# Optimization experiments

Hardware: AMD Instinct MI355X
Metric: run time of the kernel (lower is better)

## Reference

```python
import jax, jax.numpy as jnp
import numpy as np

VOCAB = 32000
HID = 512
T_IN = 128
T_OUT = 128
BATCH = 32


def gru_scan(xs, h0, W, U, bi, br):
    """Keras GRUCell (reset_after=True) over time.
    xs: [T, B, H] inputs; h0: [B, H]; W: [H, 3H]; U: [H, 3H]; bi, br: [3H].
    Returns (h_final [B,H], hs [T,B,H])."""
    # input projections for all timesteps at once
    x_proj = jnp.einsum('tbh,hg->tbg', xs, W) + bi  # [T, B, 3H]

    def step(h, xp):
        rec = h @ U + br                      # [B, 3H]
        xz, xr, xh = jnp.split(xp, 3, axis=-1)
        rz, rr, rh = jnp.split(rec, 3, axis=-1)
        z = jax.nn.sigmoid(xz + rz)
        r = jax.nn.sigmoid(xr + rr)
        hh = jnp.tanh(xh + r * rh)
        h_new = z * h + (1.0 - z) * hh
        return h_new, h_new

    h_final, hs = jax.lax.scan(step, h0, x_proj)
    return h_final, hs


def setup_inputs() -> dict:
    key = jax.random.key(0)
    ks = jax.random.split(key, 12)
    s = 0.05
    return {
        'inputs': jax.random.randint(ks[0], (BATCH, T_IN), 0, VOCAB, dtype=jnp.int64 if jax.config.jax_enable_x64 else jnp.int32),
        'emb': jax.random.normal(ks[1], (VOCAB, HID), jnp.float32) * s,
        'enc_W': jax.random.normal(ks[2], (HID, 3 * HID), jnp.float32) * s,
        'enc_U': jax.random.normal(ks[3], (HID, 3 * HID), jnp.float32) * s,
        'enc_bi': jnp.zeros((3 * HID,), jnp.float32),
        'enc_br': jnp.zeros((3 * HID,), jnp.float32),
        'dec_W': jax.random.normal(ks[4], (HID, 3 * HID), jnp.float32) * s,
        'dec_U': jax.random.normal(ks[5], (HID, 3 * HID), jnp.float32) * s,
        'dec_bi': jnp.zeros((3 * HID,), jnp.float32),
        'dec_br': jnp.zeros((3 * HID,), jnp.float32),
        'w_relu': jax.random.normal(ks[6], (HID, HID), jnp.float32) * s,
        'b_relu': jnp.zeros((HID,), jnp.float32),
        'w_out': jax.random.normal(ks[7], (HID, VOCAB), jnp.float32) * s,
        'b_out': jnp.zeros((VOCAB,), jnp.float32),
    }


def reference(inputs, emb, enc_W, enc_U, enc_bi, enc_br,
              dec_W, dec_U, dec_bi, dec_br, w_relu, b_relu, w_out, b_out):
    B = inputs.shape[0]
    # Embedding lookup: [B, T_in, H] -> time-major [T_in, B, H]
    x = jnp.transpose(emb[inputs], (1, 0, 2))
    h0 = jnp.zeros((B, HID), jnp.float32)
    # Encoder GRU -> final state
    h_enc, _ = gru_scan(x, h0, enc_W, enc_U, enc_bi, enc_br)
    # RepeatVector: decoder input is encoder state at every target step
    dec_in = jnp.broadcast_to(h_enc[None], (T_OUT, B, HID))
    # Decoder GRU with fresh zero state, return sequences
    _, hs = gru_scan(dec_in, h0, dec_W, dec_U, dec_bi, dec_br)  # [T_out, B, H]
    hs = jnp.transpose(hs, (1, 0, 2))  # [B, T_out, H]
    # TimeDistributed Dense+relu, then Dense+softmax over vocab
    h1 = jax.nn.relu(jnp.einsum('bth,hk->btk', hs, w_relu) + b_relu)
    logits = jnp.einsum('bth,hv->btv', h1, w_out) + b_out
    return jax.nn.softmax(logits, axis=-1)
```

## Files before the change

### kernel.cpp

```cpp
#include <hip/hip_runtime.h>
#include <stdint.h>

#define VOCAB 32000
#define HID   512
#define G3    1536
#define TT    128
#define BB    32
#define NROW  4096
#define NCB   250

typedef __attribute__((ext_vector_type(8))) short short8;
typedef __attribute__((ext_vector_type(4))) short short4v;
typedef __attribute__((ext_vector_type(4))) float f32x4;
typedef __attribute__((ext_vector_type(2))) unsigned long long u64x2;

__device__ __forceinline__ unsigned short f2bf(float f) {
  unsigned int u = __builtin_bit_cast(unsigned int, f);
  u += 0x7fffu + ((u >> 16) & 1u);
  return (unsigned short)(u >> 16);
}

__device__ __forceinline__ float bf2f(unsigned short s) {
  unsigned int u = ((unsigned int)s) << 16;
  return __builtin_bit_cast(float, u);
}

__device__ __forceinline__ void gload16(const void* g, void* l) {
  __builtin_amdgcn_global_load_lds(
      (const __attribute__((address_space(1))) unsigned int*)g,
      (__attribute__((address_space(3))) unsigned int*)l, 16, 0, 0);
}

__global__ void convert_bf16_k(const float* __restrict__ src,
                               unsigned short* __restrict__ dst, int n) {
  int i = (blockIdx.x * blockDim.x + threadIdx.x) * 8;
  int stride = gridDim.x * blockDim.x * 8;
  for (; i < n; i += stride) {
    float4 a = *(const float4*)(src + i);
    float4 b = *(const float4*)(src + i + 4);
    short8 o;
    o[0] = (short)f2bf(a.x); o[1] = (short)f2bf(a.y);
    o[2] = (short)f2bf(a.z); o[3] = (short)f2bf(a.w);
    o[4] = (short)f2bf(b.x); o[5] = (short)f2bf(b.y);
    o[6] = (short)f2bf(b.z); o[7] = (short)f2bf(b.w);
    *(short8*)(dst + i) = o;
  }
}

__global__ void transpose_bf16_k(const float* __restrict__ src,
                                 unsigned short* __restrict__ dst,
                                 int K, int N) {
  __shared__ float t[64][65];
  int k0 = blockIdx.x * 64, n0 = blockIdx.y * 64;
  int c = threadIdx.x & 15, rr = threadIdx.x >> 4;
#pragma unroll
  for (int i = 0; i < 4; ++i) {
    float4 v = *(const float4*)(src + (size_t)(k0 + rr + 16 * i) * N + n0 + c * 4);
    t[rr + 16 * i][c * 4 + 0] = v.x;
    t[rr + 16 * i][c * 4 + 1] = v.y;
    t[rr + 16 * i][c * 4 + 2] = v.z;
    t[rr + 16 * i][c * 4 + 3] = v.w;
  }
  __syncthreads();
#pragma unroll
  for (int i = 0; i < 4; ++i) {
    short4v o;
#pragma unroll
    for (int j = 0; j < 4; ++j) o[j] = (short)f2bf(t[c * 4 + j][rr + 16 * i]);
    *(short4v*)(dst + (size_t)(n0 + rr + 16 * i) * K + k0 + c * 4) = o;
  }
}

__global__ void embed_k(const int* __restrict__ inputs,
                        const float* __restrict__ emb,
                        unsigned short* __restrict__ xb) {
  int r = blockIdx.x;
  int t = r >> 5, b = r & 31;
  int idx = inputs[b * TT + t];
  const float* src = emb + (size_t)idx * HID;
  unsigned short* dst = xb + (size_t)r * HID;
  int j = threadIdx.x * 4;
  float4 v = *(const float4*)(src + j);
  short4v o;
  o[0] = (short)f2bf(v.x); o[1] = (short)f2bf(v.y);
  o[2] = (short)f2bf(v.z); o[3] = (short)f2bf(v.w);
  *(short4v*)(dst + j) = o;
}

template<int MODE>
__launch_bounds__(256)
__global__ void gemm_bt(const unsigned short* __restrict__ A,
                        const unsigned short* __restrict__ BT,
                        const float* __restrict__ bias,
                        void* __restrict__ Cv,
                        float* __restrict__ partials,
                        int M, int N, int K) {
  __shared__ unsigned short As[8192];
  __shared__ unsigned short Bs[8192];
  __shared__ float rsum[2][128];
  int tid = threadIdx.x;
  int l = tid & 63;
  int w = tid >> 6;
  int wm = w >> 1, wn = w & 1;

  int nwg = (int)(gridDim.x * gridDim.y);
  int id = (int)(blockIdx.y * gridDim.x + blockIdx.x);
  int nid = (id & 7) * (nwg >> 3) + (id >> 3);
  int bx = nid & 31, by = nid >> 5;
  int row0 = bx * 128;
  int col0 = by * 128;

  int sr = (w << 5) + (l >> 3);
  int sg = ((l & 7) ^ ((l >> 3) & 7)) << 3;
  const unsigned short* Ag = A  + (size_t)(row0 + sr) * K + sg;
  const unsigned short* Bg = BT + (size_t)(col0 + sr) * K + sg;

  int cA = l & 15, q = l >> 4, x7 = l & 7;
  const char* asp = (const char*)As;
  const char* bsp = (const char*)Bs;

  f32x4 acc[4][4];
#pragma unroll
  for (int m = 0; m < 4; ++m)
#pragma unroll
    for (int n = 0; n < 4; ++n) acc[m][n] = (f32x4){0.f, 0.f, 0.f, 0.f};

  for (int k0 = 0; k0 < K; k0 += 64) {
    if (k0) __syncthreads();
#pragma unroll
    for (int i = 0; i < 4; ++i) {
      gload16(Ag + (size_t)(i * 8) * K + k0, As + ((w << 2) + i) * 512);
      gload16(Bg + (size_t)(i * 8) * K + k0, Bs + ((w << 2) + i) * 512);
    }
    __syncthreads();
#pragma unroll
    for (int kk = 0; kk < 2; ++kk) {
      int sl = (((kk << 2) + q) ^ x7) << 4;
      short8 af[4], bf[4];
#pragma unroll
      for (int m = 0; m < 4; ++m)
        af[m] = *(const short8*)(asp + (wm * 64 + m * 16 + cA) * 128 + sl);
#pragma unroll
      for (int n = 0; n < 4; ++n)
        bf[n] = *(const short8*)(bsp + (wn * 64 + n * 16 + cA) * 128 + sl);
#pragma unroll
      for (int m = 0; m < 4; ++m)
#pragma unroll
        for (int n = 0; n < 4; ++n)
          acc[m][n] = __builtin_amdgcn_mfma_f32_16x16x32_bf16(af[m], bf[n],
                                                              acc[m][n], 0, 0, 0);
    }
  }

  if (MODE == 0 || MODE == 1) {
#pragma unroll
    for (int m = 0; m < 4; ++m)
#pragma unroll
      for (int n = 0; n < 4; ++n) {
        int col = col0 + wn * 64 + n * 16 + cA;
        float bv = bias[col];
#pragma unroll
        for (int r = 0; r < 4; ++r) {
          int row = row0 + wm * 64 + m * 16 + q * 4 + r;
          float v = acc[m][n][r] + bv;
          if (MODE == 0)
            ((float*)Cv)[(size_t)row * N + col] = v;
          else
            ((unsigned short*)Cv)[(size_t)row * N + col] = f2bf(fmaxf(v, 0.f));
        }
      }
  } else {
    float ps[4][4];
#pragma unroll
    for (int m = 0; m < 4; ++m)
#pragma unroll
      for (int r = 0; r < 4; ++r) ps[m][r] = 0.f;
#pragma unroll
    for (int m = 0; m < 4; ++m)
#pragma unroll
      for (int n = 0; n < 4; ++n) {
        int col = col0 + wn * 64 + n * 16 + cA;
        float bv = bias[col];
#pragma unroll
        for (int r = 0; r < 4; ++r) {
          int row = row0 + wm * 64 + m * 16 + q * 4 + r;
          float lv = acc[m][n][r] + bv;
          float v = __expf(lv);
          if (MODE == 2)
            ((float*)Cv)[(size_t)row * N + col] = v;
          else
            ((unsigned short*)Cv)[(size_t)row * N + col] = f2bf(lv);
          ps[m][r] += v;
        }
      }
#pragma unroll
    for (int mask = 1; mask < 16; mask <<= 1)
#pragma unroll
      for (int m = 0; m < 4; ++m)
#pragma unroll
        for (int r = 0; r < 4; ++r)
          ps[m][r] += __shfl_xor(ps[m][r], mask, 64);
    if (cA == 0) {
#pragma unroll
      for (int m = 0; m < 4; ++m)
#pragma unroll
        for (int r = 0; r < 4; ++r)
          rsum[wn][wm * 64 + m * 16 + q * 4 + r] = ps[m][r];
    }
    __syncthreads();
    if (tid < 128)
      partials[(size_t)by * NROW + row0 + tid] = rsum[0][tid] + rsum[1][tid];
  }
}

__launch_bounds__(256)
__global__ void gemm_small_k(const unsigned short* __restrict__ A,
                             const unsigned short* __restrict__ B,
                             const float* __restrict__ bias,
                             float* __restrict__ C,
                             int M, int N, int K) {
  __shared__ unsigned short As[64][56];
  __shared__ unsigned short Bs[64][56];
  int tid = threadIdx.x;
  int lane = tid & 63;
  int w = tid >> 6;
  int wm = w >> 1, wn = w & 1;
  int row0 = blockIdx.x * 64;
  int n0 = blockIdx.y * 64;

  f32x4 acc[2][2];
#pragma unroll
  for (int a = 0; a < 2; ++a)
#pragma unroll
    for (int c = 0; c < 2; ++c) acc[a][c] = (f32x4){0.f, 0.f, 0.f, 0.f};

  for (int k0 = 0; k0 < K; k0 += 32) {
    {
      int row = tid >> 2;
      int kg = (tid & 3) * 8;
      short8 v = {};
      if (row0 + row < M)
        v = *(const short8*)(A + (size_t)(row0 + row) * K + k0 + kg);
      *(short8*)&As[row][kg] = v;
    }
    {
      int k = tid >> 3;
      int ng = (tid & 7) * 8;
      short8 v = *(const short8*)(B + (size_t)(k0 + k) * N + n0 + ng);
#pragma unroll
      for (int qq = 0; qq < 8; ++qq) Bs[ng + qq][k] = (unsigned short)v[qq];
    }
    __syncthreads();
    int kb = (lane >> 4) * 8;
    short8 af0 = *(const short8*)&As[wm * 32 + (lane & 15)][kb];
    short8 af1 = *(const short8*)&As[wm * 32 + 16 + (lane & 15)][kb];
    short8 bf0 = *(const short8*)&Bs[wn * 32 + (lane & 15)][kb];
    short8 bf1 = *(const short8*)&Bs[wn * 32 + 16 + (lane & 15)][kb];
    acc[0][0] = __builtin_amdgcn_mfma_f32_16x16x32_bf16(af0, bf0, acc[0][0], 0, 0, 0);
    acc[0][1] = __builtin_amdgcn_mfma_f32_16x16x32_bf16(af0, bf1, acc[0][1], 0, 0, 0);
    acc[1][0] = __builtin_amdgcn_mfma_f32_16x16x32_bf16(af1, bf0, acc[1][0], 0, 0, 0);
    acc[1][1] = __builtin_amdgcn_mfma_f32_16x16x32_bf16(af1, bf1, acc[1][1], 0, 0, 0);
    __syncthreads();
  }
#pragma unroll
  for (int tm = 0; tm < 2; ++tm)
#pragma unroll
    for (int tn = 0; tn < 2; ++tn) {
      int col = n0 + wn * 32 + tn * 16 + (lane & 15);
      float bv = bias[col];
#pragma unroll
      for (int r = 0; r < 4; ++r) {
        int row = row0 + wm * 32 + tm * 16 + ((lane >> 4) * 4) + r;
        if (row < M)
          C[(size_t)row * N + col] = acc[tm][tn][r] + bv;
      }
    }
}

template<int XPT, int WRITE_ALL>
__launch_bounds__(512)
__global__ void gru_k(const float* __restrict__ U,
                      const float* __restrict__ xp,
                      const float* __restrict__ br,
                      unsigned short* __restrict__ hpub,
                      unsigned short* __restrict__ hsout,
                      unsigned int* __restrict__ flags) {
  __shared__ unsigned short ub[16 * 3 * 64 * 8];
  __shared__ unsigned short hbuf[16384];
  __shared__ float recbuf[3][32][16];
  int tid = threadIdx.x;
  int lane = tid & 63;
  int w = tid >> 6;
  int g = blockIdx.x;
  char* hbase = (char*)hbuf;

  for (int idx = tid; idx < 16 * 3 * 64 * 8; idx += 512) {
    int i = idx & 7;
    int l = (idx >> 3) & 63;
    int rem = idx >> 9;
    int nt = rem % 3;
    int ks = rem / 3;
    int k = ks * 32 + ((l >> 4) * 8) + i;
    int col = nt * 512 + g * 16 + (l & 15);
    ub[idx] = f2bf(U[(size_t)k * G3 + col]);
  }
  int b = tid >> 4, j = tid & 15;
  float br_z = br[g * 16 + j];
  float br_r = br[512 + g * 16 + j];
  float br_h = br[1024 + g * 16 + j];
  float hreg = 0.f;
  __syncthreads();

  int mt = w / 3, nt = w % 3;
  for (int t = 0; t < TT; ++t) {
    size_t xbase = ((size_t)(t * XPT + b)) * G3 + g * 16 + j;
    float xz = xp[xbase], xr = xp[xbase + 512], xh = xp[xbase + 1024];

    float rz, rr, rh;
    if (t == 0) {
      rz = 0.f; rr = 0.f; rh = 0.f;
    } else {
      {
        const unsigned long long* hr =
            (const unsigned long long*)(hpub + ((t & 1) ? 16384 : 0));
        int r = tid >> 4, s = tid & 15;
        unsigned long long av[8];
#pragma unroll
        for (int k = 0; k < 4; ++k) {
          const unsigned long long* p = hr + (size_t)r * 128 + (s + 16 * k) * 2;
          av[2 * k]     = __hip_atomic_load(p,     __ATOMIC_RELAXED,
                                            __HIP_MEMORY_SCOPE_AGENT);
          av[2 * k + 1] = __hip_atomic_load(p + 1, __ATOMIC_RELAXED,
                                            __HIP_MEMORY_SCOPE_AGENT);
        }
        int rx = (r & 7) << 4;
#pragma unroll
        for (int k = 0; k < 4; ++k) {
          int wb = (r * 1024 + (s + 16 * k) * 16) ^ rx;
          u64x2 v;
          v[0] = av[2 * k];
          v[1] = av[2 * k + 1];
          *(u64x2*)(hbase + wb) = v;
        }
      }
      __syncthreads();

      if (w < 6) {
        int arow = mt * 16 + (lane & 15);
        int rx = (arow & 7) << 4;
        int abase = arow * 1024 + (lane >> 4) * 16;
        f32x4 acc0 = (f32x4){0.f, 0.f, 0.f, 0.f};
        f32x4 acc1 = (f32x4){0.f, 0.f, 0.f, 0.f};
#pragma unroll
        for (int ks = 0; ks < 8; ++ks) {
          short8 af0 = *(const short8*)(hbase + ((abase + ks * 64) ^ rx));
          short8 af1 = *(const short8*)(hbase + ((abase + (ks + 8) * 64) ^ rx));
          short8 bf0 = *(const short8*)&ub[((ks * 3 + nt) * 64 + lane) * 8];
          short8 bf1 = *(const short8*)&ub[(((ks + 8) * 3 + nt) * 64 + lane) * 8];
          acc0 = __builtin_amdgcn_mfma_f32_16x16x32_bf16(af0, bf0, acc0, 0, 0, 0);
          acc1 = __builtin_amdgcn_mfma_f32_16x16x32_bf16(af1, bf1, acc1, 0, 0, 0);
        }
        f32x4 acc = acc0 + acc1;
#pragma unroll
        for (int r = 0; r < 4; ++r)
          recbuf[nt][mt * 16 + (lane >> 4) * 4 + r][lane & 15] = acc[r];
      }
      __syncthreads();
      rz = recbuf[0][b][j];
      rr = recbuf[1][b][j];
      rh = recbuf[2][b][j];
    }

    float z = 1.f / (1.f + __expf(-(xz + rz + br_z)));
    float rg = 1.f / (1.f + __expf(-(xr + rr + br_r)));
    float pre = xh + rg * (rh + br_h);
    pre = fminf(fmaxf(pre, -15.f), 15.f);
    float e2 = __expf(2.f * pre);
    float hh = (e2 - 1.f) / (e2 + 1.f);
    hreg = z * hreg + (1.f - z) * hh;
    unsigned short hb = f2bf(hreg);

    unsigned int hv = (unsigned int)hb;
    unsigned int p1 = (unsigned int)__shfl_xor((int)hv, 1, 64);
    unsigned long long lo = (unsigned long long)((hv & 0xffffu) | (p1 << 16));
    unsigned long long hi = (unsigned long long)__shfl_xor((int)(unsigned int)lo, 2, 64);
    if ((j & 3) == 0) {
      unsigned long long pk = (lo & 0xffffffffull) | (hi << 32);
      unsigned long long* dst = (unsigned long long*)(hpub +
          (((t + 1) & 1) ? 16384 : 0) + b * HID + g * 16 + j);
      __hip_atomic_store(dst, pk, __ATOMIC_RELAXED, __HIP_MEMORY_SCOPE_AGENT);
    }

    if (t + 1 < TT) {
      asm volatile("s_waitcnt vmcnt(0)" ::: "memory");
      __syncthreads();
      if (tid == 0)
        __hip_atomic_store(flags + g * 32, (unsigned)(t + 1),
                           __ATOMIC_RELAXED, __HIP_MEMORY_SCOPE_AGENT);
    }
    if (WRITE_ALL)
      hsout[((size_t)b * TT + t) * HID + g * 16 + j] = hb;
    if (t + 1 < TT) {
      if (lane < 32) {
        const unsigned int* fp = flags + lane * 32;
        while (__hip_atomic_load(fp, __ATOMIC_RELAXED,
                                 __HIP_MEMORY_SCOPE_AGENT) < (unsigned)(t + 1)) {}
      }
    }
  }
}

__global__ void rowsum_k(const float* __restrict__ part, float* __restrict__ inv) {
  int r = blockIdx.x * blockDim.x + threadIdx.x;
  float s = 0.f;
  for (int c = 0; c < NCB; ++c) s += part[(size_t)c * NROW + r];
  inv[r] = 1.f / s;
}

__global__ void norm_k(float* __restrict__ out, const float* __restrict__ inv) {
  const unsigned int total4 = (unsigned int)NROW * (VOCAB / 4);
  unsigned int stride = gridDim.x * blockDim.x;
  for (unsigned int i = blockIdx.x * blockDim.x + threadIdx.x; i < total4;
       i += stride) {
    unsigned int row = i / (VOCAB / 4);
    float s = inv[row];
    float4* p = (float4*)out + i;
    float4 v = *p;
    v.x *= s; v.y *= s; v.z *= s; v.w *= s;
    *p = v;
  }
}

__global__ void norm2_k(const unsigned short* __restrict__ lg,
                        const float* __restrict__ inv,
                        float* __restrict__ out) {
  const unsigned int total8 = (unsigned int)NROW * (VOCAB / 8);
  unsigned int stride = gridDim.x * blockDim.x;
  for (unsigned int i = blockIdx.x * blockDim.x + threadIdx.x; i < total8;
       i += stride) {
    unsigned int row = i / (VOCAB / 8);
    float s = inv[row];
    short8 v = *(const short8*)(lg + (size_t)i * 8);
    float4 a, b;
    a.x = __expf(bf2f((unsigned short)v[0])) * s;
    a.y = __expf(bf2f((unsigned short)v[1])) * s;
    a.z = __expf(bf2f((unsigned short)v[2])) * s;
    a.w = __expf(bf2f((unsigned short)v[3])) * s;
    b.x = __expf(bf2f((unsigned short)v[4])) * s;
    b.y = __expf(bf2f((unsigned short)v[5])) * s;
    b.z = __expf(bf2f((unsigned short)v[6])) * s;
    b.w = __expf(bf2f((unsigned short)v[7])) * s;
    *(float4*)(out + (size_t)i * 8) = a;
    *(float4*)(out + (size_t)i * 8 + 4) = b;
  }
}

extern "C" void kernel_launch(void* const* d_in, const int* in_sizes, int n_in,
                              void* d_out, int out_size, void* d_ws, size_t ws_size,
                              hipStream_t stream) {
  const int*   inputs = (const int*)d_in[0];
  const float* emb    = (const float*)d_in[1];
  const float* encW   = (const float*)d_in[2];
  const float* encU   = (const float*)d_in[3];
  const float* enc_bi = (const float*)d_in[4];
  const float* enc_br = (const float*)d_in[5];
  const float* decW   = (const float*)d_in[6];
  const float* decU   = (const float*)d_in[7];
  const float* dec_bi = (const float*)d_in[8];
  const float* dec_br = (const float*)d_in[9];
  const float* w_relu = (const float*)d_in[10];
  const float* b_relu = (const float*)d_in[11];
  const float* w_out  = (const float*)d_in[12];
  const float* b_out  = (const float*)d_in[13];

  char* ws = (char*)d_ws;
  const size_t o_xproj  = 0;
  const size_t o_xb     = 25165824;
  const size_t o_encWbT = 29360128;
  const size_t o_decWb  = 30932992;
  const size_t o_wrelubT= 32505856;
  const size_t o_woutbT = 33030144;
  const size_t o_decxp  = 65798144;
  const size_t o_hsb    = 65994752;
  const size_t o_h1b    = 70189056;
  const size_t o_part   = 74383360;
  const size_t o_inv    = 82575360;
  const size_t o_hpubE  = 82591744;
  const size_t o_hpubD  = 82657280;
  const size_t o_logit  = 82722816;
  const size_t need_big = o_logit + (size_t)NROW * VOCAB * 2;

  float*          xproj   = (float*)(ws + o_xproj);
  unsigned short* xb      = (unsigned short*)(ws + o_xb);
  unsigned short* encWbT  = (unsigned short*)(ws + o_encWbT);
  unsigned short* decWb   = (unsigned short*)(ws + o_decWb);
  unsigned short* wrelubT = (unsigned short*)(ws + o_wrelubT);
  unsigned short* woutbT  = (unsigned short*)(ws + o_woutbT);
  float*          decxp   = (float*)(ws + o_decxp);
  unsigned short* hsb     = (unsigned short*)(ws + o_hsb);
  unsigned short* h1b     = (unsigned short*)(ws + o_h1b);
  float*          part    = (float*)(ws + o_part);
  float*          inv     = (float*)(ws + o_inv);
  unsigned short* hpubE   = (unsigned short*)(ws + o_hpubE);
  unsigned short* hpubD   = (unsigned short*)(ws + o_hpubD);
  unsigned short* logit   = (unsigned short*)(ws + o_logit);
  unsigned int*   flagsE  = (unsigned int*)(ws + o_part);
  unsigned int*   flagsD  = (unsigned int*)(ws + o_part + 4096);

  (void)hipMemsetAsync(ws + o_part, 0, 8192, stream);
  (void)hipMemsetAsync(ws + o_hpubE, 0, 65536 * 2, stream);

  transpose_bf16_k<<<dim3(8, 24), 256, 0, stream>>>(encW, encWbT, HID, G3);
  transpose_bf16_k<<<dim3(8, 8), 256, 0, stream>>>(w_relu, wrelubT, HID, HID);
  transpose_bf16_k<<<dim3(8, 500), 256, 0, stream>>>(w_out, woutbT, HID, VOCAB);
  convert_bf16_k<<<384, 256, 0, stream>>>(decW, decWb, 512 * G3);

  embed_k<<<4096, 128, 0, stream>>>(inputs, emb, xb);

  gemm_bt<0><<<dim3(32, 12), 256, 0, stream>>>(xb, encWbT, enc_bi, xproj,
                                               nullptr, NROW, G3, HID);
  gru_k<32, 0><<<32, 512, 0, stream>>>(encU, xproj, enc_br, hpubE, nullptr, flagsE);

  gemm_small_k<<<dim3(1, 24), 256, 0, stream>>>(hpubE, decWb, dec_bi, decxp,
                                                BB, G3, HID);
  gru_k<0, 1><<<32, 512, 0, stream>>>(decU, decxp, dec_br, hpubD, hsb, flagsD);

  gemm_bt<1><<<dim3(32, 4), 256, 0, stream>>>(hsb, wrelubT, b_relu, h1b,
                                              nullptr, NROW, HID, HID);

  if (ws_size >= need_big) {
    gemm_bt<3><<<dim3(32, NCB), 256, 0, stream>>>(h1b, woutbT, b_out, logit,
                                                  part, NROW, VOCAB, HID);
    rowsum_k<<<16, 256, 0, stream>>>(part, inv);
    norm2_k<<<2048, 256, 0, stream>>>(logit, inv, (float*)d_out);
  } else {
    gemm_bt<2><<<dim3(32, NCB), 256, 0, stream>>>(h1b, woutbT, b_out, d_out,
                                                  part, NROW, VOCAB, HID);
    rowsum_k<<<16, 256, 0, stream>>>(part, inv);
    norm_k<<<2048, 256, 0, stream>>>((float*)d_out, inv);
  }
}
```

Before: 1.289 ms.

## Overlap GRU recurrences with weight conversion and output GEMMs via persistent fused kernels

```diff
diff --git a/kernel.cpp b/kernel.cpp
--- a/kernel.cpp
+++ b/kernel.cpp
@@ -19,32 +19,26 @@
   u += 0x7fffu + ((u >> 16) & 1u);
   return (unsigned short)(u >> 16);
 }
-
 __device__ __forceinline__ float bf2f(unsigned short s) {
   unsigned int u = ((unsigned int)s) << 16;
   return __builtin_bit_cast(float, u);
 }
-
 __device__ __forceinline__ void gload16(const void* g, void* l) {
   __builtin_amdgcn_global_load_lds(
       (const __attribute__((address_space(1))) unsigned int*)g,
       (__attribute__((address_space(3))) unsigned int*)l, 16, 0, 0);
 }
-
-__global__ void convert_bf16_k(const float* __restrict__ src,
-                               unsigned short* __restrict__ dst, int n) {
-  int i = (blockIdx.x * blockDim.x + threadIdx.x) * 8;
-  int stride = gridDim.x * blockDim.x * 8;
-  for (; i < n; i += stride) {
-    float4 a = *(const float4*)(src + i);
-    float4 b = *(const float4*)(src + i + 4);
-    short8 o;
-    o[0] = (short)f2bf(a.x); o[1] = (short)f2bf(a.y);
-    o[2] = (short)f2bf(a.z); o[3] = (short)f2bf(a.w);
-    o[4] = (short)f2bf(b.x); o[5] = (short)f2bf(b.y);
-    o[6] = (short)f2bf(b.z); o[7] = (short)f2bf(b.w);
-    *(short8*)(dst + i) = o;
-  }
+__device__ __forceinline__ unsigned long long AL64(const unsigned long long* p) {
+  return __hip_atomic_load(p, __ATOMIC_RELAXED, __HIP_MEMORY_SCOPE_AGENT);
+}
+__device__ __forceinline__ unsigned int AL32(const unsigned int* p) {
+  return __hip_atomic_load(p, __ATOMIC_RELAXED, __HIP_MEMORY_SCOPE_AGENT);
+}
+__device__ __forceinline__ void AS64(unsigned long long* p, unsigned long long v) {
+  __hip_atomic_store(p, v, __ATOMIC_RELAXED, __HIP_MEMORY_SCOPE_AGENT);
+}
+__device__ __forceinline__ void AS32(unsigned int* p, unsigned int v) {
+  __hip_atomic_store(p, v, __ATOMIC_RELAXED, __HIP_MEMORY_SCOPE_AGENT);
 }
 
 __global__ void transpose_bf16_k(const float* __restrict__ src,
@@ -87,34 +81,28 @@
   *(short4v*)(dst + j) = o;
 }
 
-template<int MODE>
 __launch_bounds__(256)
-__global__ void gemm_bt(const unsigned short* __restrict__ A,
-                        const unsigned short* __restrict__ BT,
-                        const float* __restrict__ bias,
-                        void* __restrict__ Cv,
-                        float* __restrict__ partials,
-                        int M, int N, int K) {
+__global__ void gemm_bt0(const unsigned short* __restrict__ A,
+                         const unsigned short* __restrict__ BT,
+                         const float* __restrict__ bias,
+                         float* __restrict__ C,
+                         int M, int N, int K) {
   __shared__ unsigned short As[8192];
   __shared__ unsigned short Bs[8192];
-  __shared__ float rsum[2][128];
   int tid = threadIdx.x;
   int l = tid & 63;
   int w = tid >> 6;
   int wm = w >> 1, wn = w & 1;
-
   int nwg = (int)(gridDim.x * gridDim.y);
   int id = (int)(blockIdx.y * gridDim.x + blockIdx.x);
   int nid = (id & 7) * (nwg >> 3) + (id >> 3);
   int bx = nid & 31, by = nid >> 5;
-  int row0 = bx * 128;
-  int col0 = by * 128;
+  int row0 = bx * 128, col0 = by * 128;
 
   int sr = (w << 5) + (l >> 3);
   int sg = ((l & 7) ^ ((l >> 3) & 7)) << 3;
   const unsigned short* Ag = A  + (size_t)(row0 + sr) * K + sg;
   const unsigned short* Bg = BT + (size_t)(col0 + sr) * K + sg;
-
   int cA = l & 15, q = l >> 4, x7 = l & 7;
   const char* asp = (const char*)As;
   const char* bsp = (const char*)Bs;
@@ -151,66 +139,18 @@
                                                               acc[m][n], 0, 0, 0);
     }
   }
-
-  if (MODE == 0 || MODE == 1) {
-#pragma unroll
-    for (int m = 0; m < 4; ++m)
-#pragma unroll
-      for (int n = 0; n < 4; ++n) {
-        int col = col0 + wn * 64 + n * 16 + cA;
-        float bv = bias[col];
-#pragma unroll
-        for (int r = 0; r < 4; ++r) {
-          int row = row0 + wm * 64 + m * 16 + q * 4 + r;
-          float v = acc[m][n][r] + bv;
-          if (MODE == 0)
-            ((float*)Cv)[(size_t)row * N + col] = v;
-          else
-            ((unsigned short*)Cv)[(size_t)row * N + col] = f2bf(fmaxf(v, 0.f));
-        }
-      }
-  } else {
-    float ps[4][4];
-#pragma unroll
-    for (int m = 0; m < 4; ++m)
-#pragma unroll
-      for (int r = 0; r < 4; ++r) ps[m][r] = 0.f;
-#pragma unroll
-    for (int m = 0; m < 4; ++m)
-#pragma unroll
-      for (int n = 0; n < 4; ++n) {
-        int col = col0 + wn * 64 + n * 16 + cA;
-        float bv = bias[col];
-#pragma unroll
-        for (int r = 0; r < 4; ++r) {
-          int row = row0 + wm * 64 + m * 16 + q * 4 + r;
-          float lv = acc[m][n][r] + bv;
-          float v = __expf(lv);
-          if (MODE == 2)
-            ((float*)Cv)[(size_t)row * N + col] = v;
-          else
-            ((unsigned short*)Cv)[(size_t)row * N + col] = f2bf(lv);
-          ps[m][r] += v;
-        }
-      }
-#pragma unroll
-    for (int mask = 1; mask < 16; mask <<= 1)
-#pragma unroll
-      for (int m = 0; m < 4; ++m)
-#pragma unroll
-        for (int r = 0; r < 4; ++r)
-          ps[m][r] += __shfl_xor(ps[m][r], mask, 64);
-    if (cA == 0) {
-#pragma unroll
-      for (int m = 0; m < 4; ++m)
-#pragma unroll
-        for (int r = 0; r < 4; ++r)
-          rsum[wn][wm * 64 + m * 16 + q * 4 + r] = ps[m][r];
-    }
-    __syncthreads();
-    if (tid < 128)
-      partials[(size_t)by * NROW + row0 + tid] = rsum[0][tid] + rsum[1][tid];
-  }
+#pragma unroll
+  for (int m = 0; m < 4; ++m)
+#pragma unroll
+    for (int n = 0; n < 4; ++n) {
+      int col = col0 + wn * 64 + n * 16 + cA;
+      float bv = bias[col];
+#pragma unroll
+      for (int r = 0; r < 4; ++r) {
+        int row = row0 + wm * 64 + m * 16 + q * 4 + r;
+        C[(size_t)row * N + col] = acc[m][n][r] + bv;
+      }
+    }
 }
 
 __launch_bounds__(256)
@@ -227,13 +167,11 @@
   int wm = w >> 1, wn = w & 1;
   int row0 = blockIdx.x * 64;
   int n0 = blockIdx.y * 64;
-
   f32x4 acc[2][2];
 #pragma unroll
   for (int a = 0; a < 2; ++a)
 #pragma unroll
     for (int c = 0; c < 2; ++c) acc[a][c] = (f32x4){0.f, 0.f, 0.f, 0.f};
-
   for (int k0 = 0; k0 < K; k0 += 32) {
     {
       int row = tid >> 2;
@@ -278,21 +216,19 @@
 }
 
 template<int XPT, int WRITE_ALL>
-__launch_bounds__(512)
-__global__ void gru_k(const float* __restrict__ U,
-                      const float* __restrict__ xp,
-                      const float* __restrict__ br,
-                      unsigned short* __restrict__ hpub,
-                      unsigned short* __restrict__ hsout,
-                      unsigned int* __restrict__ flags) {
-  __shared__ unsigned short ub[16 * 3 * 64 * 8];
-  __shared__ unsigned short hbuf[16384];
-  __shared__ float recbuf[3][32][16];
+__device__ void gru_body(char* smem, const float* __restrict__ U,
+                         const float* __restrict__ xp, const float* __restrict__ br,
+                         unsigned short* __restrict__ hpub,
+                         unsigned long long* __restrict__ hsq,
+                         unsigned int* __restrict__ flags,
+                         unsigned int* __restrict__ wprog) {
+  unsigned short* ub = (unsigned short*)smem;
+  char* hbase = smem + 49152;
+  float (*recbuf)[32][16] = (float (*)[32][16])(smem + 81920);
   int tid = threadIdx.x;
   int lane = tid & 63;
   int w = tid >> 6;
   int g = blockIdx.x;
-  char* hbase = (char*)hbuf;
 
   for (int idx = tid; idx < 16 * 3 * 64 * 8; idx += 512) {
     int i = idx & 7;
@@ -328,10 +264,8 @@
 #pragma unroll
         for (int k = 0; k < 4; ++k) {
           const unsigned long long* p = hr + (size_t)r * 128 + (s + 16 * k) * 2;
-          av[2 * k]     = __hip_atomic_load(p,     __ATOMIC_RELAXED,
-                                            __HIP_MEMORY_SCOPE_AGENT);
-          av[2 * k + 1] = __hip_atomic_load(p + 1, __ATOMIC_RELAXED,
-                                            __HIP_MEMORY_SCOPE_AGENT);
+          av[2 * k] = AL64(p);
+          av[2 * k + 1] = AL64(p + 1);
         }
         int rx = (r & 7) << 4;
 #pragma unroll
@@ -383,29 +317,277 @@
     unsigned int hv = (unsigned int)hb;
     unsigned int p1 = (unsigned int)__shfl_xor((int)hv, 1, 64);
     unsigned long long lo = (unsigned long long)((hv & 0xffffu) | (p1 << 16));
-    unsigned long long hi = (unsigned long long)__shfl_xor((int)(unsigned int)lo, 2, 64);
+    unsigned long long hi =
+        (unsigned long long)(unsigned int)__shfl_xor((int)(unsigned int)lo, 2, 64);
+    unsigned long long pk = (lo & 0xffffffffull) | (hi << 32);
     if ((j & 3) == 0) {
-      unsigned long long pk = (lo & 0xffffffffull) | (hi << 32);
-      unsigned long long* dst = (unsigned long long*)(hpub +
-          (((t + 1) & 1) ? 16384 : 0) + b * HID + g * 16 + j);
-      __hip_atomic_store(dst, pk, __ATOMIC_RELAXED, __HIP_MEMORY_SCOPE_AGENT);
-    }
-
-    if (t + 1 < TT) {
+      AS64((unsigned long long*)(hpub + (((t + 1) & 1) ? 16384 : 0) +
+                                 b * HID + g * 16 + j), pk);
+      if (WRITE_ALL)
+        AS64(hsq + ((size_t)t * 32 + b) * 128 + g * 4 + (j >> 2), pk);
+    }
+
+    if (WRITE_ALL || t + 1 < TT) {
       asm volatile("s_waitcnt vmcnt(0)" ::: "memory");
       __syncthreads();
       if (tid == 0)
-        __hip_atomic_store(flags + g * 32, (unsigned)(t + 1),
-                           __ATOMIC_RELAXED, __HIP_MEMORY_SCOPE_AGENT);
-    }
-    if (WRITE_ALL)
-      hsout[((size_t)b * TT + t) * HID + g * 16 + j] = hb;
-    if (t + 1 < TT) {
+        AS32(flags + g * 32, (unsigned)(t + 1));
       if (lane < 32) {
         const unsigned int* fp = flags + lane * 32;
-        while (__hip_atomic_load(fp, __ATOMIC_RELAXED,
-                                 __HIP_MEMORY_SCOPE_AGENT) < (unsigned)(t + 1)) {}
-      }
+        while (AL32(fp) < (unsigned)(t + 1)) {}
+      }
+      if (WRITE_ALL && g == 0 && w == 0 && lane == 0)
+        AS32(wprog, (unsigned)(t + 1));
+    }
+  }
+}
+
+template<int MODE>
+__device__ void eng_tile(char* sm, int tid8, int rt, int ct, bool live,
+                         const unsigned long long* __restrict__ Aq,
+                         const unsigned short* __restrict__ BT,
+                         const float* __restrict__ bias,
+                         unsigned long long* __restrict__ outq,
+                         unsigned short* __restrict__ outl,
+                         float* __restrict__ partials,
+                         unsigned int* __restrict__ h1done) {
+  unsigned short* As = (unsigned short*)sm;
+  unsigned short* Bs = (unsigned short*)(sm + 16384);
+  float* rsum = (float*)(sm + 32768);
+  int l = tid8 & 63, w = tid8 >> 6;
+  int wm = w >> 1, wn = w & 1;
+  int row0 = rt * 128, col0 = ct * 128;
+  int sr = (w << 5) + (l >> 3);
+  int sg = ((l & 7) ^ ((l >> 3) & 7)) << 3;
+  int cA = l & 15, q = l >> 6 ? 0 : (l >> 4);
+  q = l >> 4;
+  int x7 = l & 7;
+  const char* asp = (const char*)As;
+  const char* bsp = (const char*)Bs;
+  const unsigned long long* Ag = Aq + (size_t)(row0 + sr) * 128 + (sg >> 2);
+  const unsigned short* Bg = BT + (size_t)(col0 + sr) * 512 + sg;
+
+  f32x4 acc[4][4];
+#pragma unroll
+  for (int m = 0; m < 4; ++m)
+#pragma unroll
+    for (int n = 0; n < 4; ++n) acc[m][n] = (f32x4){0.f, 0.f, 0.f, 0.f};
+
+  for (int k0 = 0; k0 < 512; k0 += 64) {
+    if (k0) __syncthreads();
+#pragma unroll
+    for (int i = 0; i < 4; ++i) {
+      const unsigned long long* p = Ag + (size_t)(i * 8) * 128 + (k0 >> 2);
+      unsigned long long a0 = AL64(p);
+      unsigned long long a1 = AL64(p + 1);
+      u64x2 v2; v2[0] = a0; v2[1] = a1;
+      *(u64x2*)((char*)As + (w * 4 + i) * 1024 + l * 16) = v2;
+      gload16(Bg + (size_t)(i * 8) * 512 + k0, Bs + ((w << 2) + i) * 512);
+    }
+    __syncthreads();
+#pragma unroll
+    for (int kk = 0; kk < 2; ++kk) {
+      int sl = (((kk << 2) + q) ^ x7) << 4;
+      short8 af[4], bf[4];
+#pragma unroll
+      for (int m = 0; m < 4; ++m)
+        af[m] = *(const short8*)(asp + (wm * 64 + m * 16 + cA) * 128 + sl);
+#pragma unroll
+      for (int n = 0; n < 4; ++n)
+        bf[n] = *(const short8*)(bsp + (wn * 64 + n * 16 + cA) * 128 + sl);
+#pragma unroll
+      for (int m = 0; m < 4; ++m)
+#pragma unroll
+        for (int n = 0; n < 4; ++n)
+          acc[m][n] = __builtin_amdgcn_mfma_f32_16x16x32_bf16(af[m], bf[n],
+                                                              acc[m][n], 0, 0, 0);
+    }
+  }
+
+  if (MODE == 1) {
+#pragma unroll
+    for (int m = 0; m < 4; ++m)
+#pragma unroll
+      for (int n = 0; n < 4; ++n) {
+        int col = col0 + wn * 64 + n * 16 + cA;
+        float bv = bias[col];
+#pragma unroll
+        for (int r = 0; r < 4; ++r) {
+          int row = row0 + wm * 64 + m * 16 + q * 4 + r;
+          unsigned int hv = (unsigned int)f2bf(fmaxf(acc[m][n][r] + bv, 0.f));
+          unsigned int p1 = (unsigned int)__shfl_xor((int)hv, 1, 64);
+          unsigned long long lo =
+              (unsigned long long)((hv & 0xffffu) | (p1 << 16));
+          unsigned long long hi = (unsigned long long)(unsigned int)
+              __shfl_xor((int)(unsigned int)lo, 2, 64);
+          if (live && (cA & 3) == 0)
+            AS64(outq + (size_t)row * 128 + (col >> 2),
+                 (lo & 0xffffffffull) | (hi << 32));
+        }
+      }
+    __syncthreads();
+    if (live && tid8 == 0)
+      __hip_atomic_fetch_add(h1done + rt * 32, 1u, __ATOMIC_RELAXED,
+                             __HIP_MEMORY_SCOPE_AGENT);
+  } else {
+    float ps[4][4];
+#pragma unroll
+    for (int m = 0; m < 4; ++m)
+#pragma unroll
+      for (int r = 0; r < 4; ++r) ps[m][r] = 0.f;
+#pragma unroll
+    for (int m = 0; m < 4; ++m)
+#pragma unroll
+      for (int n = 0; n < 4; ++n) {
+        int col = col0 + wn * 64 + n * 16 + cA;
+        float bv = bias[col];
+#pragma unroll
+        for (int r = 0; r < 4; ++r) {
+          int row = row0 + wm * 64 + m * 16 + q * 4 + r;
+          float lv = acc[m][n][r] + bv;
+          float ev = __expf(lv);
+          if (live)
+            outl[(size_t)row * VOCAB + col] = f2bf(lv);
+          ps[m][r] += ev;
+        }
+      }
+#pragma unroll
+    for (int mask = 1; mask < 16; mask <<= 1)
+#pragma unroll
+      for (int m = 0; m < 4; ++m)
+#pragma unroll
+        for (int r = 0; r < 4; ++r)
+          ps[m][r] += __shfl_xor(ps[m][r], mask, 64);
+    if (cA == 0) {
+#pragma unroll
+      for (int m = 0; m < 4; ++m)
+#pragma unroll
+        for (int r = 0; r < 4; ++r)
+          rsum[wn * 128 + wm * 64 + m * 16 + q * 4 + r] = ps[m][r];
+    }
+    __syncthreads();
+    if (live && tid8 < 128)
+      partials[(size_t)ct * NROW + row0 + tid8] = rsum[tid8] + rsum[128 + tid8];
+  }
+}
+
+__device__ void tr_tile(char* sm, int tid8, const float* __restrict__ src,
+                        unsigned short* __restrict__ dst,
+                        int K, int N, int k0, int n0) {
+  float (*t)[65] = (float (*)[65])sm;
+  int c = tid8 & 15, rr = tid8 >> 4;
+#pragma unroll
+  for (int i = 0; i < 4; ++i) {
+    float4 v = *(const float4*)(src + (size_t)(k0 + rr + 16 * i) * N + n0 + c * 4);
+    t[rr + 16 * i][c * 4 + 0] = v.x;
+    t[rr + 16 * i][c * 4 + 1] = v.y;
+    t[rr + 16 * i][c * 4 + 2] = v.z;
+    t[rr + 16 * i][c * 4 + 3] = v.w;
+  }
+  __syncthreads();
+#pragma unroll
+  for (int i = 0; i < 4; ++i) {
+    short4v o;
+#pragma unroll
+    for (int j = 0; j < 4; ++j) o[j] = (short)f2bf(t[c * 4 + j][rr + 16 * i]);
+    *(short4v*)(dst + (size_t)(n0 + rr + 16 * i) * K + k0 + c * 4) = o;
+  }
+}
+
+__launch_bounds__(512)
+__global__ void enc_fused_k(const float* __restrict__ U,
+                            const float* __restrict__ xp,
+                            const float* __restrict__ br,
+                            unsigned short* __restrict__ hpub,
+                            unsigned int* __restrict__ flags,
+                            const float* __restrict__ w_out,
+                            unsigned short* __restrict__ woutbT,
+                            const float* __restrict__ w_relu,
+                            unsigned short* __restrict__ wrelubT,
+                            const float* __restrict__ decW,
+                            unsigned short* __restrict__ decWb) {
+  __shared__ char smem[88064];
+  if (blockIdx.x < 32) {
+    gru_body<32, 0>(smem, U, xp, br, hpub, nullptr, flags, nullptr);
+    return;
+  }
+  int tid = threadIdx.x;
+  int wid = (int)blockIdx.x - 32;
+  int eng = tid >> 8, tid8 = tid & 255;
+  char* sm = smem + eng * 36864;
+  for (int it = 0; it < 10; ++it) {
+    int tk = wid * 2 + eng + it * 448;
+    if (tk < 4000) {
+      tr_tile(sm, tid8, w_out, woutbT, 512, VOCAB, (tk & 7) * 64, (tk >> 3) * 64);
+    } else if (tk < 4064) {
+      int t2 = tk - 4000;
+      tr_tile(sm, tid8, w_relu, wrelubT, 512, 512, (t2 & 7) * 64, (t2 >> 3) * 64);
+    } else if (tk < 4448) {
+      int c = tk - 4064;
+      int base = c * 2048 + tid8 * 8;
+      float4 a = *(const float4*)(decW + base);
+      float4 bq = *(const float4*)(decW + base + 4);
+      short8 o;
+      o[0] = (short)f2bf(a.x); o[1] = (short)f2bf(a.y);
+      o[2] = (short)f2bf(a.z); o[3] = (short)f2bf(a.w);
+      o[4] = (short)f2bf(bq.x); o[5] = (short)f2bf(bq.y);
+      o[6] = (short)f2bf(bq.z); o[7] = (short)f2bf(bq.w);
+      *(short8*)(decWb + base) = o;
+      __syncthreads();
+    } else {
+      __syncthreads();
+    }
+  }
+}
+
+__launch_bounds__(512)
+__global__ void dec_fused_k(const float* __restrict__ U,
+                            const float* __restrict__ xp,
+                            const float* __restrict__ br,
+                            unsigned short* __restrict__ hpub,
+                            unsigned long long* __restrict__ hsq,
+                            unsigned int* __restrict__ flags,
+                            unsigned int* __restrict__ wprog,
+                            unsigned int* __restrict__ h1done,
+                            const unsigned short* __restrict__ wrelubT,
+                            const float* __restrict__ b_relu,
+                            unsigned long long* __restrict__ h1q,
+                            const unsigned short* __restrict__ woutbT,
+                            const float* __restrict__ b_out,
+                            unsigned short* __restrict__ logit,
+                            float* __restrict__ part) {
+  __shared__ char smem[88064];
+  if (blockIdx.x < 32) {
+    gru_body<0, 1>(smem, U, xp, br, hpub, hsq, flags, wprog);
+    return;
+  }
+  int tid = threadIdx.x;
+  int wid = (int)blockIdx.x - 32;
+  int eng = tid >> 8, tid8 = tid & 255;
+  int l = tid8 & 63;
+  char* sm = smem + eng * 36864;
+  for (int it = 0; it < 19; ++it) {
+    int tk = wid * 2 + eng + it * 448;
+    bool live = tk < 8128;
+    int rt = live ? (tk / 254) : 0;
+    int u = live ? (tk % 254) : 254;
+    if (live && u < 4) {
+      if (l == 0) {
+        while ((int)AL32(wprog) < 4 * rt + 4) __builtin_amdgcn_s_sleep(8);
+      }
+      __builtin_amdgcn_sched_barrier(0);
+      eng_tile<1>(sm, tid8, rt, u, true, hsq, wrelubT, b_relu,
+                  h1q, nullptr, nullptr, h1done);
+    } else {
+      int ct = live ? (u - 4) : 0;
+      if (live) {
+        if (l == 0) {
+          while (AL32(h1done + rt * 32) < 4u) __builtin_amdgcn_s_sleep(8);
+        }
+        __builtin_amdgcn_sched_barrier(0);
+      }
+      eng_tile<3>(sm, tid8, rt, ct, live, h1q, woutbT, b_out,
+                  nullptr, logit, part, nullptr);
     }
   }
 }
@@ -417,30 +599,19 @@
   inv[r] = 1.f / s;
 }
 
-__global__ void norm_k(float* __restrict__ out, const float* __restrict__ inv) {
-  const unsigned int total4 = (unsigned int)NROW * (VOCAB / 4);
-  unsigned int stride = gridDim.x * blockDim.x;
-  for (unsigned int i = blockIdx.x * blockDim.x + threadIdx.x; i < total4;
-       i += stride) {
-    unsigned int row = i / (VOCAB / 4);
-    float s = inv[row];
-    float4* p = (float4*)out + i;
-    float4 v = *p;
-    v.x *= s; v.y *= s; v.z *= s; v.w *= s;
-    *p = v;
-  }
-}
-
 __global__ void norm2_k(const unsigned short* __restrict__ lg,
                         const float* __restrict__ inv,
                         float* __restrict__ out) {
-  const unsigned int total8 = (unsigned int)NROW * (VOCAB / 8);
+  const unsigned int C8 = VOCAB / 8;
+  const unsigned int total8 = (unsigned int)NROW * C8;
   unsigned int stride = gridDim.x * blockDim.x;
   for (unsigned int i = blockIdx.x * blockDim.x + threadIdx.x; i < total8;
        i += stride) {
-    unsigned int row = i / (VOCAB / 8);
-    float s = inv[row];
+    unsigned int r = i / C8;
+    unsigned int c8 = i - r * C8;
+    float s = inv[r];
     short8 v = *(const short8*)(lg + (size_t)i * 8);
+    size_t obase = ((size_t)((r & 31) * TT + (r >> 5))) * VOCAB + (size_t)c8 * 8;
     float4 a, b;
     a.x = __expf(bf2f((unsigned short)v[0])) * s;
     a.y = __expf(bf2f((unsigned short)v[1])) * s;
@@ -450,8 +621,8 @@
     b.y = __expf(bf2f((unsigned short)v[5])) * s;
     b.z = __expf(bf2f((unsigned short)v[6])) * s;
     b.w = __expf(bf2f((unsigned short)v[7])) * s;
-    *(float4*)(out + (size_t)i * 8) = a;
-    *(float4*)(out + (size_t)i * 8 + 4) = b;
+    *(float4*)(out + obase) = a;
+    *(float4*)(out + obase + 4) = b;
   }
 }
 
@@ -488,7 +659,6 @@
   const size_t o_hpubE  = 82591744;
   const size_t o_hpubD  = 82657280;
   const size_t o_logit  = 82722816;
-  const size_t need_big = o_logit + (size_t)NROW * VOCAB * 2;
 
   float*          xproj   = (float*)(ws + o_xproj);
   unsigned short* xb      = (unsigned short*)(ws + o_xb);
@@ -497,46 +667,40 @@
   unsigned short* wrelubT = (unsigned short*)(ws + o_wrelubT);
   unsigned short* woutbT  = (unsigned short*)(ws + o_woutbT);
   float*          decxp   = (float*)(ws + o_decxp);
-  unsigned short* hsb     = (unsigned short*)(ws + o_hsb);
-  unsigned short* h1b     = (unsigned short*)(ws + o_h1b);
+  unsigned long long* hsq = (unsigned long long*)(ws + o_hsb);
+  unsigned long long* h1q = (unsigned long long*)(ws + o_h1b);
   float*          part    = (float*)(ws + o_part);
   float*          inv     = (float*)(ws + o_inv);
   unsigned short* hpubE   = (unsigned short*)(ws + o_hpubE);
   unsigned short* hpubD   = (unsigned short*)(ws + o_hpubD);
   unsigned short* logit   = (unsigned short*)(ws + o_logit);
   unsigned int*   flagsE  = (unsigned int*)(ws + o_part);
-  unsigned int*   flagsD  = (unsigned int*)(ws + o_part + 4096);
+  unsigned int*   flagsD  = (unsigned int*)(ws + o_xb);
+  unsigned int*   wprog   = (unsigned int*)(ws + o_xb + 4096);
+  unsigned int*   h1done  = (unsigned int*)(ws + o_xb + 8192);
 
   (void)hipMemsetAsync(ws + o_part, 0, 8192, stream);
-  (void)hipMemsetAsync(ws + o_hpubE, 0, 65536 * 2, stream);
+  (void)hipMemsetAsync(ws + o_hpubE, 0, 131072, stream);
 
   transpose_bf16_k<<<dim3(8, 24), 256, 0, stream>>>(encW, encWbT, HID, G3);
-  transpose_bf16_k<<<dim3(8, 8), 256, 0, stream>>>(w_relu, wrelubT, HID, HID);
-  transpose_bf16_k<<<dim3(8, 500), 256, 0, stream>>>(w_out, woutbT, HID, VOCAB);
-  convert_bf16_k<<<384, 256, 0, stream>>>(decW, decWb, 512 * G3);
-
   embed_k<<<4096, 128, 0, stream>>>(inputs, emb, xb);
 
-  gemm_bt<0><<<dim3(32, 12), 256, 0, stream>>>(xb, encWbT, enc_bi, xproj,
-                                               nullptr, NROW, G3, HID);
-  gru_k<32, 0><<<32, 512, 0, stream>>>(encU, xproj, enc_br, hpubE, nullptr, flagsE);
+  gemm_bt0<<<dim3(32, 12), 256, 0, stream>>>(xb, encWbT, enc_bi, xproj,
+                                             NROW, G3, HID);
+  (void)hipMemsetAsync(ws + o_xb, 0, 16384, stream);
+
+  enc_fused_k<<<256, 512, 0, stream>>>(encU, xproj, enc_br, hpubE, flagsE,
+                                       w_out, woutbT, w_relu, wrelubT,
+                                       decW, decWb);
 
   gemm_small_k<<<dim3(1, 24), 256, 0, stream>>>(hpubE, decWb, dec_bi, decxp,
                                                 BB, G3, HID);
-  gru_k<0, 1><<<32, 512, 0, stream>>>(decU, decxp, dec_br, hpubD, hsb, flagsD);
-
-  gemm_bt<1><<<dim3(32, 4), 256, 0, stream>>>(hsb, wrelubT, b_relu, h1b,
-                                              nullptr, NROW, HID, HID);
-
-  if (ws_size >= need_big) {
-    gemm_bt<3><<<dim3(32, NCB), 256, 0, stream>>>(h1b, woutbT, b_out, logit,
-                                                  part, NROW, VOCAB, HID);
-    rowsum_k<<<16, 256, 0, stream>>>(part, inv);
-    norm2_k<<<2048, 256, 0, stream>>>(logit, inv, (float*)d_out);
-  } else {
-    gemm_bt<2><<<dim3(32, NCB), 256, 0, stream>>>(h1b, woutbT, b_out, d_out,
-                                                  part, NROW, VOCAB, HID);
-    rowsum_k<<<16, 256, 0, stream>>>(part, inv);
-    norm_k<<<2048, 256, 0, stream>>>((float*)d_out, inv);
-  }
-}
+
+  dec_fused_k<<<256, 512, 0, stream>>>(decU, decxp, dec_br, hpubD, hsq,
+                                       flagsD, wprog, h1done,
+                                       wrelubT, b_relu, h1q,
+                                       woutbT, b_out, logit, part);
+
+  rowsum_k<<<16, 256, 0, stream>>>(part, inv);
+  norm2_k<<<2048, 256, 0, stream>>>(logit, inv, (float*)d_out);
+}
```

New measurement: 1.379 ms. 7.0% more time.
